# Kernel optimization log

Hardware: AMD Instinct MI355X
Metric: run time of the kernel (lower is better)

## Reference

```python
import jax, jax.numpy as jnp
import numpy as np

ALPHA = 0.2  # LeakyReLU negative slope
NEG = -9e15


def gat_layer(h, adj, W, a):
    # Faithful to the torch GAT: e_ij = leakyrelu(a^T [Wh_i || Wh_j])
    # = leakyrelu(a_src . Wh_i + a_dst . Wh_j); avoids the NxNx2F materialization.
    Wh = h @ W                              # [N, F]
    Fo = W.shape[1]
    a_src, a_dst = a[:Fo, 0], a[Fo:, 0]
    e = jax.nn.leaky_relu(
        (Wh @ a_src)[:, None] + (Wh @ a_dst)[None, :], negative_slope=ALPHA
    )                                        # [N, N]
    e = jnp.where(adj > 0, e, NEG)
    att = jax.nn.softmax(e, axis=1)          # dropout p=0 (eval)
    return jax.nn.elu(att @ Wh)


def gru_cell(x, h, W_ih, W_hh, b_ih, b_hh):
    # PyTorch GRUCell semantics.
    gi = x @ W_ih.T + b_ih                   # [N, 3F]
    gh = h @ W_hh.T + b_hh
    i_r, i_z, i_n = jnp.split(gi, 3, axis=1)
    h_r, h_z, h_n = jnp.split(gh, 3, axis=1)
    r = jax.nn.sigmoid(i_r + h_r)
    z = jax.nn.sigmoid(i_z + h_z)
    n = jnp.tanh(i_n + r * h_n)
    return (1.0 - z) * n + z * h


def setup_inputs() -> dict:
    key = jax.random.key(0)
    ks = jax.random.split(key, 10)
    N, nfeat, nhid, nout = 8192, 256, 128, 128
    x = jax.random.normal(ks[0], (N, nfeat), dtype=jnp.float32)
    # sparse random binary adjacency (~32 avg degree) + self loops
    adj = (jax.random.uniform(ks[1], (N, N)) < 0.004).astype(jnp.float32)
    adj = jnp.maximum(adj, jnp.eye(N, dtype=jnp.float32))
    h_prev = jnp.zeros((N, nout), dtype=jnp.float32)

    def xavier(k, shape, gain=1.414):
        fan_in, fan_out = shape[0], shape[1]
        b = gain * np.sqrt(6.0 / (fan_in + fan_out))
        return jax.random.uniform(k, shape, jnp.float32, -b, b)

    W1 = xavier(ks[2], (nfeat, nhid))
    a1 = xavier(ks[3], (2 * nhid, 1))
    W2 = xavier(ks[4], (nhid, nout))
    a2 = xavier(ks[5], (2 * nout, 1))
    s = 1.0 / np.sqrt(nout)
    W_ih = jax.random.uniform(ks[6], (3 * nout, nout), jnp.float32, -s, s)
    W_hh = jax.random.uniform(ks[7], (3 * nout, nout), jnp.float32, -s, s)
    b_ih = jax.random.uniform(ks[8], (3 * nout,), jnp.float32, -s, s)
    b_hh = jax.random.uniform(ks[9], (3 * nout,), jnp.float32, -s, s)
    return {"x": x, "adj": adj, "h_prev": h_prev, "W1": W1, "a1": a1,
            "W2": W2, "a2": a2, "W_ih": W_ih, "W_hh": W_hh,
            "b_ih": b_ih, "b_hh": b_hh}


def reference(x, adj, h_prev, W1, a1, W2, a2, W_ih, W_hh, b_ih, b_hh):
    x1 = gat_layer(x, adj, W1, a1)
    h_spat = gat_layer(x1, adj, W2, a2)
    return gru_cell(h_spat, h_prev, W_ih, W_hh, b_ih, b_hh)
```

## Files before the change

### kernel.cpp

```cpp
#include <hip/hip_runtime.h>
#include <math.h>

#define N_NODES 8192
#define CAP 128
#define LRELU_ALPHA 0.2f

typedef float v4f __attribute__((ext_vector_type(4)));

template <int K>
__device__ __forceinline__ void gemm_from_lds(
    int r0, int t, const float* As, const float* __restrict__ W,
    const float* __restrict__ a, float* __restrict__ Wh, float* __restrict__ src,
    float* __restrict__ dst, float (*red)[4][2]) {
  int c = t & 127, half = t >> 7;
  float acc[4] = {0.f, 0.f, 0.f, 0.f};
  const float* Asl = As + (half * 4) * K;
#pragma unroll 8
  for (int k = 0; k < K; k++) {
    float wv = W[k * 128 + c];
#pragma unroll
    for (int r = 0; r < 4; r++) acc[r] += Asl[r * K + k] * wv;
  }
  float as = a[c], ad = a[128 + c];
  int wv_id = t >> 6, lane = t & 63;
#pragma unroll
  for (int r = 0; r < 4; r++) {
    int row = half * 4 + r;
    Wh[(size_t)(r0 + row) * 128 + c] = acc[r];
    float s = acc[r] * as, d = acc[r] * ad;
#pragma unroll
    for (int off = 32; off; off >>= 1) {
      s += __shfl_xor(s, off);
      d += __shfl_xor(d, off);
    }
    if (lane == 0) { red[wv_id][r][0] = s; red[wv_id][r][1] = d; }
  }
  __syncthreads();
  if (t < 8) {
    int wa = (t < 4) ? 0 : 2, rr = t & 3;
    src[r0 + t] = red[wa][rr][0] + red[wa + 1][rr][0];
    dst[r0 + t] = red[wa][rr][1] + red[wa + 1][rr][1];
  }
}

__device__ __forceinline__ void agg_to_lds(
    int i, int q, int t, const float* __restrict__ Wh, const float* __restrict__ src,
    const float* __restrict__ dst, const int* __restrict__ idxbuf,
    const int* __restrict__ counts, float* tile, int* jn, float* w, float* redm, float* reds,
    float* accs) {
  int lane = t & 63, wv = t >> 6;
  int c = counts[i];
  float si = src[i];
  float e = -1e30f;
  if (t < c) {
    int j = idxbuf[(size_t)i * CAP + t];
    jn[t] = j;
    float x = si + dst[j];
    e = x > 0.f ? x : LRELU_ALPHA * x;
  }
  float m = e;
#pragma unroll
  for (int off = 32; off; off >>= 1) m = fmaxf(m, __shfl_xor(m, off));
  if (lane == 0) redm[wv] = m;
  __syncthreads();
  float M = fmaxf(fmaxf(redm[0], redm[1]), fmaxf(redm[2], redm[3]));
  float ex = 0.f;
  if (t < c) {
    ex = expf(e - M);
    w[t] = ex;
  }
  float s = ex;
#pragma unroll
  for (int off = 32; off; off >>= 1) s += __shfl_xor(s, off);
  if (lane == 0) reds[wv] = s;
  __syncthreads();
  float inv = 1.f / (reds[0] + reds[1] + reds[2] + reds[3]);
  int col = t & 127, half = t >> 7;
  float acc = 0.f;
  int k = half;
  for (; k + 6 < c; k += 8)
    acc += w[k] * Wh[(size_t)jn[k] * 128 + col] + w[k + 2] * Wh[(size_t)jn[k + 2] * 128 + col] +
           w[k + 4] * Wh[(size_t)jn[k + 4] * 128 + col] +
           w[k + 6] * Wh[(size_t)jn[k + 6] * 128 + col];
  for (; k < c; k += 2) acc += w[k] * Wh[(size_t)jn[k] * 128 + col];
  if (half == 0) accs[col] = acc;
  __syncthreads();
  if (half == 1) {
    float a = (accs[col] + acc) * inv;
    tile[q * 128 + col] = a > 0.f ? a : expf(a) - 1.f;
  }
  __syncthreads();
}

__global__ __launch_bounds__(256) void kA(
    const float* __restrict__ adj, int* __restrict__ idxbuf, int* __restrict__ counts,
    const float* __restrict__ x, const float* __restrict__ W1, const float* __restrict__ a1,
    float* __restrict__ Wh1, float* __restrict__ src1, float* __restrict__ dst1,
    const float* __restrict__ Wi, const float* __restrict__ Whm, float* __restrict__ WiT,
    float* __restrict__ WhT) {
  __shared__ float As[8 * 256];
  __shared__ float red[4][4][2];
  __shared__ int jn[CAP];
  __shared__ int cnt;
  int t = threadIdx.x, b = blockIdx.x;
  if (b < N_NODES) {
    if (t == 0) cnt = 0;
    __syncthreads();
    const v4f* row = (const v4f*)(adj + (size_t)b * N_NODES);
    v4f v[8];
#pragma unroll
    for (int u = 0; u < 8; u++) v[u] = __builtin_nontemporal_load(row + t + 256 * u);
#pragma unroll
    for (int u = 0; u < 8; u++) {
      int n = (v[u].x > 0.f) + (v[u].y > 0.f) + (v[u].z > 0.f) + (v[u].w > 0.f);
      if (n) {
        int p = atomicAdd(&cnt, n);
        int j0 = (t + 256 * u) * 4;
        if (v[u].x > 0.f) { if (p < CAP) jn[p] = j0;     p++; }
        if (v[u].y > 0.f) { if (p < CAP) jn[p] = j0 + 1; p++; }
        if (v[u].z > 0.f) { if (p < CAP) jn[p] = j0 + 2; p++; }
        if (v[u].w > 0.f) { if (p < CAP) jn[p] = j0 + 3; p++; }
      }
    }
    __syncthreads();
    int c = cnt > CAP ? CAP : cnt;
    if (t < c) idxbuf[(size_t)b * CAP + t] = jn[t];
    if (t == 0) counts[b] = c;
  } else if (b < N_NODES + 1024) {
    int tile = b - N_NODES;
    const float4* Ab4 = (const float4*)(x + (size_t)tile * 8 * 256);
    float4* As4 = (float4*)As;
#pragma unroll
    for (int l = t; l < 8 * 256 / 4; l += 256) As4[l] = Ab4[l];
    __syncthreads();
    gemm_from_lds<256>(tile * 8, t, As, W1, a1, Wh1, src1, dst1, red);
  } else {
    for (int n = (b - N_NODES - 1024) * 256 + t; n < 384 * 128; n += 64 * 256) {
      int r = n >> 7, c = n & 127;
      WiT[c * 384 + r] = Wi[n];
      WhT[c * 384 + r] = Whm[n];
    }
  }
}

__global__ __launch_bounds__(256) void kB(
    const float* __restrict__ Wh1, const float* __restrict__ src1,
    const float* __restrict__ dst1, const int* __restrict__ idxbuf,
    const int* __restrict__ counts, const float* __restrict__ W2, const float* __restrict__ a2,
    float* __restrict__ Wh2, float* __restrict__ src2, float* __restrict__ dst2) {
  __shared__ float tile[8 * 128];
  __shared__ float red[4][4][2];
  __shared__ int jn[CAP];
  __shared__ float w[CAP];
  __shared__ float redm[4];
  __shared__ float reds[4];
  __shared__ float accs[128];
  int t = threadIdx.x, b = blockIdx.x;
  int i0 = b * 8;
#pragma unroll 1
  for (int q = 0; q < 8; q++)
    agg_to_lds(i0 + q, q, t, Wh1, src1, dst1, idxbuf, counts, tile, jn, w, redm, reds, accs);
  gemm_from_lds<128>(i0, t, tile, W2, a2, Wh2, src2, dst2, red);
}

__global__ __launch_bounds__(256) void kC(
    const float* __restrict__ Wh2, const float* __restrict__ src2,
    const float* __restrict__ dst2, const int* __restrict__ idxbuf,
    const int* __restrict__ counts, const float* __restrict__ hprev,
    const float* __restrict__ WiT, const float* __restrict__ WhT,
    const float* __restrict__ b_ih, const float* __restrict__ b_hh, float* __restrict__ outp) {
  __shared__ float tile[8 * 128];
  __shared__ float hs[8 * 128];
  __shared__ int jn[CAP];
  __shared__ float w[CAP];
  __shared__ float redm[4];
  __shared__ float reds[4];
  __shared__ float accs[128];
  int t = threadIdx.x, b = blockIdx.x;
  int i0 = b * 8;
  ((float4*)hs)[t] = ((const float4*)(hprev + (size_t)i0 * 128))[t];
#pragma unroll 1
  for (int q = 0; q < 8; q++)
    agg_to_lds(i0 + q, q, t, Wh2, src2, dst2, idxbuf, counts, tile, jn, w, redm, reds, accs);
  int c = t & 127, half = t >> 7;
  const float* xsl = tile + half * 4 * 128;
  const float* hsl = hs + half * 4 * 128;
  float rg[4], zg[4];
  {
    float ai[4] = {0.f}, ah[4] = {0.f};
#pragma unroll 4
    for (int k = 0; k < 128; k++) {
      float wi = WiT[k * 384 + c], wh = WhT[k * 384 + c];
#pragma unroll
      for (int r = 0; r < 4; r++) { ai[r] += xsl[r * 128 + k] * wi; ah[r] += hsl[r * 128 + k] * wh; }
    }
    float bi = b_ih[c], bh = b_hh[c];
#pragma unroll
    for (int r = 0; r < 4; r++) rg[r] = 1.f / (1.f + expf(-(ai[r] + bi + ah[r] + bh)));
  }
  {
    float ai[4] = {0.f}, ah[4] = {0.f};
#pragma unroll 4
    for (int k = 0; k < 128; k++) {
      float wi = WiT[k * 384 + 128 + c], wh = WhT[k * 384 + 128 + c];
#pragma unroll
      for (int r = 0; r < 4; r++) { ai[r] += xsl[r * 128 + k] * wi; ah[r] += hsl[r * 128 + k] * wh; }
    }
    float bi = b_ih[128 + c], bh = b_hh[128 + c];
#pragma unroll
    for (int r = 0; r < 4; r++) zg[r] = 1.f / (1.f + expf(-(ai[r] + bi + ah[r] + bh)));
  }
  {
    float ai[4] = {0.f}, ah[4] = {0.f};
#pragma unroll 4
    for (int k = 0; k < 128; k++) {
      float wi = WiT[k * 384 + 256 + c], wh = WhT[k * 384 + 256 + c];
#pragma unroll
      for (int r = 0; r < 4; r++) { ai[r] += xsl[r * 128 + k] * wi; ah[r] += hsl[r * 128 + k] * wh; }
    }
    float bi = b_ih[256 + c], bh = b_hh[256 + c];
#pragma unroll
    for (int r = 0; r < 4; r++) {
      float n = tanhf(ai[r] + bi + rg[r] * (ah[r] + bh));
      outp[(size_t)(i0 + half * 4 + r) * 128 + c] =
          (1.f - zg[r]) * n + zg[r] * hsl[r * 128 + c];
    }
  }
}

extern "C" void kernel_launch(void* const* d_in, const int* in_sizes, int n_in,
                              void* d_out, int out_size, void* d_ws, size_t ws_size,
                              hipStream_t stream) {
  const float* x     = (const float*)d_in[0];
  const float* adj   = (const float*)d_in[1];
  const float* hprev = (const float*)d_in[2];
  const float* W1    = (const float*)d_in[3];
  const float* a1    = (const float*)d_in[4];
  const float* W2    = (const float*)d_in[5];
  const float* a2    = (const float*)d_in[6];
  const float* Wi    = (const float*)d_in[7];
  const float* Whm   = (const float*)d_in[8];
  const float* b_ih  = (const float*)d_in[9];
  const float* b_hh  = (const float*)d_in[10];
  float* outp = (float*)d_out;

  char* p = (char*)d_ws;
  float* Wh1    = (float*)p; p += (size_t)N_NODES * 128 * 4;
  float* Wh2    = (float*)p; p += (size_t)N_NODES * 128 * 4;
  float* src1   = (float*)p; p += (size_t)N_NODES * 4;
  float* dst1   = (float*)p; p += (size_t)N_NODES * 4;
  float* src2   = (float*)p; p += (size_t)N_NODES * 4;
  float* dst2   = (float*)p; p += (size_t)N_NODES * 4;
  float* WiT    = (float*)p; p += (size_t)384 * 128 * 4;
  float* WhT    = (float*)p; p += (size_t)384 * 128 * 4;
  int*   counts = (int*)p;   p += (size_t)N_NODES * 4;
  int*   idxbuf = (int*)p;   p += (size_t)N_NODES * CAP * 4;

  kA<<<N_NODES + 1024 + 64, 256, 0, stream>>>(adj, idxbuf, counts, x, W1, a1, Wh1, src1, dst1,
                                              Wi, Whm, WiT, WhT);
  kB<<<N_NODES / 8, 256, 0, stream>>>(Wh1, src1, dst1, idxbuf, counts, W2, a2, Wh2, src2, dst2);
  kC<<<N_NODES / 8, 256, 0, stream>>>(Wh2, src2, dst2, idxbuf, counts, hprev, WiT, WhT, b_ih,
                                      b_hh, outp);
}
```

Measured before the change: 473.9 us.

## Aggregate two nodes per block iteration with float4 neighbor gathers

The sparse attention aggregation in kB and kC now handles two nodes at once, each on one 128-thread half of the block, which halves the number of sequential iterations and barriers. The neighbor feature gather uses float4 loads, with four slots splitting the neighbor list and a reduction through shared memory. Each node's softmax now covers at most 128 neighbors using half the threads, which matches the CAP of 128. Shared memory use grows somewhat because of the per-slot partial-sum buffers.

Measured after the change: 452.4 us. -4.5%, faster.

```diff
diff --git a/kernel.cpp b/kernel.cpp
--- a/kernel.cpp
+++ b/kernel.cpp
@@ -43,52 +43,64 @@
   }
 }
 
-__device__ __forceinline__ void agg_to_lds(
-    int i, int q, int t, const float* __restrict__ Wh, const float* __restrict__ src,
+__device__ __forceinline__ void agg_pair(
+    int i0, int s, int t, const float* __restrict__ Wh, const float* __restrict__ src,
     const float* __restrict__ dst, const int* __restrict__ idxbuf,
-    const int* __restrict__ counts, float* tile, int* jn, float* w, float* redm, float* reds,
-    float* accs) {
-  int lane = t & 63, wv = t >> 6;
+    const int* __restrict__ counts, float* tile, int (*jn)[128], float (*w)[128],
+    float (*redm)[2], float (*reds)[2], float (*accs)[4][128]) {
+  int half = t >> 7;
+  int u = t & 127;
+  int wv = (t >> 6) & 1;
+  int i = i0 + s * 2 + half;
   int c = counts[i];
   float si = src[i];
   float e = -1e30f;
-  if (t < c) {
-    int j = idxbuf[(size_t)i * CAP + t];
-    jn[t] = j;
-    float x = si + dst[j];
-    e = x > 0.f ? x : LRELU_ALPHA * x;
+  if (u < c) {
+    int j = idxbuf[(size_t)i * CAP + u];
+    jn[half][u] = j;
+    float xv = si + dst[j];
+    e = xv > 0.f ? xv : LRELU_ALPHA * xv;
   }
   float m = e;
 #pragma unroll
   for (int off = 32; off; off >>= 1) m = fmaxf(m, __shfl_xor(m, off));
-  if (lane == 0) redm[wv] = m;
-  __syncthreads();
-  float M = fmaxf(fmaxf(redm[0], redm[1]), fmaxf(redm[2], redm[3]));
+  if ((t & 63) == 0) redm[half][wv] = m;
+  __syncthreads();
+  float M = fmaxf(redm[half][0], redm[half][1]);
   float ex = 0.f;
-  if (t < c) {
+  if (u < c) {
     ex = expf(e - M);
-    w[t] = ex;
-  }
-  float s = ex;
-#pragma unroll
-  for (int off = 32; off; off >>= 1) s += __shfl_xor(s, off);
-  if (lane == 0) reds[wv] = s;
-  __syncthreads();
-  float inv = 1.f / (reds[0] + reds[1] + reds[2] + reds[3]);
-  int col = t & 127, half = t >> 7;
-  float acc = 0.f;
-  int k = half;
-  for (; k + 6 < c; k += 8)
-    acc += w[k] * Wh[(size_t)jn[k] * 128 + col] + w[k + 2] * Wh[(size_t)jn[k + 2] * 128 + col] +
-           w[k + 4] * Wh[(size_t)jn[k + 4] * 128 + col] +
-           w[k + 6] * Wh[(size_t)jn[k + 6] * 128 + col];
-  for (; k < c; k += 2) acc += w[k] * Wh[(size_t)jn[k] * 128 + col];
-  if (half == 0) accs[col] = acc;
-  __syncthreads();
-  if (half == 1) {
-    float a = (accs[col] + acc) * inv;
-    tile[q * 128 + col] = a > 0.f ? a : expf(a) - 1.f;
-  }
+    w[half][u] = ex;
+  }
+  float ss = ex;
+#pragma unroll
+  for (int off = 32; off; off >>= 1) ss += __shfl_xor(ss, off);
+  if ((t & 63) == 0) reds[half][wv] = ss;
+  __syncthreads();
+  float inv = 1.f / (reds[half][0] + reds[half][1]);
+  int slot = (t >> 5) & 3, col4 = t & 31;
+  const float4* Wh4 = (const float4*)Wh;
+  float ax = 0.f, ay = 0.f, az = 0.f, aw = 0.f;
+  int k = slot;
+  for (; k + 4 < c; k += 8) {
+    float w0 = w[half][k], w1 = w[half][k + 4];
+    float4 v0 = Wh4[(size_t)jn[half][k] * 32 + col4];
+    float4 v1 = Wh4[(size_t)jn[half][k + 4] * 32 + col4];
+    ax += w0 * v0.x + w1 * v1.x;
+    ay += w0 * v0.y + w1 * v1.y;
+    az += w0 * v0.z + w1 * v1.z;
+    aw += w0 * v0.w + w1 * v1.w;
+  }
+  if (k < c) {
+    float w0 = w[half][k];
+    float4 v0 = Wh4[(size_t)jn[half][k] * 32 + col4];
+    ax += w0 * v0.x; ay += w0 * v0.y; az += w0 * v0.z; aw += w0 * v0.w;
+  }
+  *(float4*)&accs[half][slot][col4 * 4] = make_float4(ax, ay, az, aw);
+  __syncthreads();
+  float r = accs[half][0][u] + accs[half][1][u] + accs[half][2][u] + accs[half][3][u];
+  r *= inv;
+  tile[(s * 2 + half) * 128 + u] = r > 0.f ? r : expf(r) - 1.f;
   __syncthreads();
 }
 
@@ -150,16 +162,16 @@
     float* __restrict__ Wh2, float* __restrict__ src2, float* __restrict__ dst2) {
   __shared__ float tile[8 * 128];
   __shared__ float red[4][4][2];
-  __shared__ int jn[CAP];
-  __shared__ float w[CAP];
-  __shared__ float redm[4];
-  __shared__ float reds[4];
-  __shared__ float accs[128];
+  __shared__ int jn[2][128];
+  __shared__ float w[2][128];
+  __shared__ float redm[2][2];
+  __shared__ float reds[2][2];
+  __shared__ float accs[2][4][128];
   int t = threadIdx.x, b = blockIdx.x;
   int i0 = b * 8;
 #pragma unroll 1
-  for (int q = 0; q < 8; q++)
-    agg_to_lds(i0 + q, q, t, Wh1, src1, dst1, idxbuf, counts, tile, jn, w, redm, reds, accs);
+  for (int s = 0; s < 4; s++)
+    agg_pair(i0, s, t, Wh1, src1, dst1, idxbuf, counts, tile, jn, w, redm, reds, accs);
   gemm_from_lds<128>(i0, t, tile, W2, a2, Wh2, src2, dst2, red);
 }
 
@@ -171,17 +183,17 @@
     const float* __restrict__ b_ih, const float* __restrict__ b_hh, float* __restrict__ outp) {
   __shared__ float tile[8 * 128];
   __shared__ float hs[8 * 128];
-  __shared__ int jn[CAP];
-  __shared__ float w[CAP];
-  __shared__ float redm[4];
-  __shared__ float reds[4];
-  __shared__ float accs[128];
+  __shared__ int jn[2][128];
+  __shared__ float w[2][128];
+  __shared__ float redm[2][2];
+  __shared__ float reds[2][2];
+  __shared__ float accs[2][4][128];
   int t = threadIdx.x, b = blockIdx.x;
   int i0 = b * 8;
   ((float4*)hs)[t] = ((const float4*)(hprev + (size_t)i0 * 128))[t];
 #pragma unroll 1
-  for (int q = 0; q < 8; q++)
-    agg_to_lds(i0 + q, q, t, Wh2, src2, dst2, idxbuf, counts, tile, jn, w, redm, reds, accs);
+  for (int s = 0; s < 4; s++)
+    agg_pair(i0, s, t, Wh2, src2, dst2, idxbuf, counts, tile, jn, w, redm, reds, accs);
   int c = t & 127, half = t >> 7;
   const float* xsl = tile + half * 4 * 128;
   const float* hsl = hs + half * 4 * 128;
```
